# Kernel tuning notes

Hardware: AMD Instinct MI355X
Metric: run time of the kernel (lower is better)

Reference implementation:

```python
import jax, jax.numpy as jnp
import numpy as np

H, W = 128, 128  # image_shape


def setup_inputs() -> dict:
    key = jax.random.key(0)
    Y = jax.random.uniform(key, (32, H * W), dtype=jnp.float32)
    return {"Y": Y}


def reference(Y):
    # Binarize and reshape to images: [B, H, W]
    Yb = (Y > 0.5).astype(jnp.float32).reshape(-1, H, W)

    # DP over rows: heights[i, j] = number of consecutive 1s ending at row i in column j
    def step(h, row):
        h = (h + 1.0) * row
        return h, h

    _, heights = jax.lax.scan(step, jnp.zeros((Yb.shape[0], W), Yb.dtype),
                              jnp.swapaxes(Yb, 0, 1))
    heights = jnp.swapaxes(heights, 0, 1)  # [B, H, W]

    # Largest rectangle in histogram, vectorized over all rows.
    # For bar j: left[j] = prev index k with h[k] < h[j] (else -1),
    #            right[j] = next index k with h[k] < h[j] (else W).
    # This matches the monotonic-stack scan (pops while h[stack[-1]] >= h[i]).
    idx = jnp.arange(W)
    kk = idx[:, None]  # candidate index k (axis -2)
    jj = idx[None, :]  # bar index j (axis -1)
    less = heights[..., :, None] < heights[..., None, :]  # [B, H, W, W]; less[k, j] = h[k] < h[j]
    left = jnp.max(jnp.where(less & (kk < jj), kk, -1), axis=-2)   # [B, H, W]
    right = jnp.min(jnp.where(less & (kk > jj), kk, W), axis=-2)   # [B, H, W]

    area = heights * (right - left - 1).astype(heights.dtype)  # [B, H, W]
    maxarea = jnp.max(area, axis=(1, 2))  # [B]; all-zero image -> 0, matching original
    return maxarea.astype(jnp.int32)[:, None]  # [B, 1]
```

## Files before the change

kernel.cpp:

```cpp
#include <hip/hip_runtime.h>

static constexpr int H = 128;
static constexpr int W = 128;
static constexpr int B = 32;
static constexpr int RPB = 4;
static constexpr int WIN = RPB + 31;
static constexpr int GPB = H / RPB;

__global__ __launch_bounds__(64) void lr_rows(const float* __restrict__ Y,
                                              int* __restrict__ partials,
                                              int* __restrict__ out,
                                              int use_atomic) {
    const int blk = blockIdx.x;
    const int b = blk >> 5;
    const int rg = blk & (GPB - 1);
    const int r_top = rg * RPB + (RPB - 1);
    const int l = threadIdx.x;
    const float* __restrict__ yA = Y + (size_t)b * H * W + l;
    const float* __restrict__ yB = yA + 64;

    unsigned long long mA = 0ULL, mB = 0ULL;
    #pragma unroll
    for (int k = 0; k < WIN; ++k) {
        int t = r_top - k; t = t < 0 ? 0 : t;
        if (yA[(size_t)t * W] > 0.5f) mA |= (1ULL << k);
        if (yB[(size_t)t * W] > 0.5f) mB |= (1ULL << k);
    }
    if (r_top < WIN - 1) {
        const unsigned long long keep = (2ULL << r_top) - 1ULL;
        mA &= keep; mB &= keep;
    }

    int hA[RPB], hB[RPB];
    #pragma unroll
    for (int s = 0; s < RPB; ++s) {
        const int r = r_top - s;
        int a = __builtin_ctzll(~(mA >> s));
        if (a == WIN - s && r - a >= 0) {
            int t = r - a;
            while (t >= 0 && yA[(size_t)t * W] > 0.5f) { ++a; --t; }
        }
        int c = __builtin_ctzll(~(mB >> s));
        if (c == WIN - s && r - c >= 0) {
            int t = r - c;
            while (t >= 0 && yB[(size_t)t * W] > 0.5f) { ++c; --t; }
        }
        hA[s] = a; hB[s] = c;
    }

    int hm = 0;
    #pragma unroll
    for (int s = 0; s < RPB; ++s) hm = max(hm, max(hA[s], hB[s]));
    #pragma unroll
    for (int off = 32; off > 0; off >>= 1)
        hm = max(hm, __shfl_xor(hm, off, 64));

    unsigned long long loA[RPB] = {}, hiA[RPB] = {};
    unsigned long long loB[RPB] = {}, hiB[RPB] = {};
    for (int t = 1; t <= hm; ++t) {
        #pragma unroll
        for (int s = 0; s < RPB; ++s) {
            const unsigned long long lo = __ballot(hA[s] < t);
            const unsigned long long hi = __ballot(hB[s] < t);
            if (hA[s] == t) { loA[s] = lo; hiA[s] = hi; }
            if (hB[s] == t) { loB[s] = lo; hiB[s] = hi; }
        }
    }

    int acc = 0;
    #pragma unroll
    for (int s = 0; s < RPB; ++s) {
        {
            const unsigned long long below = loA[s] & ((1ULL << l) - 1ULL);
            const unsigned long long above = loA[s] & ~((2ULL << l) - 1ULL);
            const int left  = below ? 63 - __builtin_clzll(below) : -1;
            const int right = above ? __builtin_ctzll(above)
                                    : (hiA[s] ? 64 + __builtin_ctzll(hiA[s]) : W);
            acc = max(acc, hA[s] * (right - left - 1));
        }
        {
            const unsigned long long below = hiB[s] & ((1ULL << l) - 1ULL);
            const unsigned long long above = hiB[s] & ~((2ULL << l) - 1ULL);
            const int left  = below ? 64 + 63 - __builtin_clzll(below)
                                    : (loB[s] ? 63 - __builtin_clzll(loB[s]) : -1);
            const int right = above ? 64 + __builtin_ctzll(above) : W;
            acc = max(acc, hB[s] * (right - left - 1));
        }
    }

    #pragma unroll
    for (int off = 32; off > 0; off >>= 1)
        acc = max(acc, __shfl_xor(acc, off, 64));
    if (l == 0) {
        if (use_atomic) atomicMax(&out[b], acc);
        else partials[blk] = acc;
    }
}

__global__ __launch_bounds__(64) void lr_reduce(const int* __restrict__ partials,
                                                int* __restrict__ out) {
    const int b = blockIdx.x;
    const int j = threadIdx.x;
    int v = (j < GPB) ? partials[b * GPB + j] : 0;
    #pragma unroll
    for (int off = 32; off > 0; off >>= 1)
        v = max(v, __shfl_xor(v, off, 64));
    if (j == 0) out[b] = v;
}

extern "C" void kernel_launch(void* const* d_in, const int* in_sizes, int n_in,
                              void* d_out, int out_size, void* d_ws, size_t ws_size,
                              hipStream_t stream) {
    const float* Y = (const float*)d_in[0];
    int* out = (int*)d_out;

    if (ws_size >= (size_t)(B * GPB) * sizeof(int)) {
        int* partials = (int*)d_ws;
        lr_rows<<<B * GPB, 64, 0, stream>>>(Y, partials, out, 0);
        lr_reduce<<<B, 64, 0, stream>>>(partials, out);
    } else {
        hipMemsetAsync(out, 0, (size_t)out_size * sizeof(int), stream);
        lr_rows<<<B * GPB, 64, 0, stream>>>(Y, nullptr, out, 1);
    }
}
```

Measured before the change: 13.10 us.

## Fuse row kernel and reduction into one block per image with shared-memory max

Replaces the two-kernel scheme (1024 single-wave blocks writing partials, then a reduce kernel) with one kernel launching one 1024-thread block per image. Each of its 16 waves handles 8 rows, and the per-image max is combined through shared memory and __syncthreads. This removes the second launch and the global partials round trip, and halves the window overlap per row, cutting redundant loads. In exchange only 32 blocks run, so fewer CUs are used, and each wave does twice the ballot work serially.

```diff
diff --git a/kernel.cpp b/kernel.cpp
--- a/kernel.cpp
+++ b/kernel.cpp
@@ -3,19 +3,18 @@
 static constexpr int H = 128;
 static constexpr int W = 128;
 static constexpr int B = 32;
-static constexpr int RPB = 4;
-static constexpr int WIN = RPB + 31;
-static constexpr int GPB = H / RPB;
+static constexpr int RPW = 8;
+static constexpr int WIN = RPW + 31;
+static constexpr int WAVES = H / RPW;
+static constexpr int NT = WAVES * 64;
 
-__global__ __launch_bounds__(64) void lr_rows(const float* __restrict__ Y,
-                                              int* __restrict__ partials,
-                                              int* __restrict__ out,
-                                              int use_atomic) {
-    const int blk = blockIdx.x;
-    const int b = blk >> 5;
-    const int rg = blk & (GPB - 1);
-    const int r_top = rg * RPB + (RPB - 1);
-    const int l = threadIdx.x;
+__global__ __launch_bounds__(NT) void lr_batch(const float* __restrict__ Y,
+                                               int* __restrict__ out) {
+    const int b = blockIdx.x;
+    const int tid = threadIdx.x;
+    const int w = tid >> 6;
+    const int l = tid & 63;
+    const int r_top = w * RPW + (RPW - 1);
     const float* __restrict__ yA = Y + (size_t)b * H * W + l;
     const float* __restrict__ yB = yA + 64;
 
@@ -31,9 +30,9 @@
         mA &= keep; mB &= keep;
     }
 
-    int hA[RPB], hB[RPB];
+    int hA[RPW], hB[RPW];
     #pragma unroll
-    for (int s = 0; s < RPB; ++s) {
+    for (int s = 0; s < RPW; ++s) {
         const int r = r_top - s;
         int a = __builtin_ctzll(~(mA >> s));
         if (a == WIN - s && r - a >= 0) {
@@ -48,64 +47,62 @@
         hA[s] = a; hB[s] = c;
     }
 
-    int hm = 0;
+    int acc = 0;
     #pragma unroll
-    for (int s = 0; s < RPB; ++s) hm = max(hm, max(hA[s], hB[s]));
-    #pragma unroll
-    for (int off = 32; off > 0; off >>= 1)
-        hm = max(hm, __shfl_xor(hm, off, 64));
+    for (int g = 0; g < 2; ++g) {
+        const int s0 = g * 4;
+        int hm = 0;
+        #pragma unroll
+        for (int s = 0; s < 4; ++s) hm = max(hm, max(hA[s0 + s], hB[s0 + s]));
+        #pragma unroll
+        for (int off = 32; off > 0; off >>= 1)
+            hm = max(hm, __shfl_xor(hm, off, 64));
 
-    unsigned long long loA[RPB] = {}, hiA[RPB] = {};
-    unsigned long long loB[RPB] = {}, hiB[RPB] = {};
-    for (int t = 1; t <= hm; ++t) {
+        unsigned long long loA[4] = {}, hiA[4] = {};
+        unsigned long long loB[4] = {}, hiB[4] = {};
+        for (int t = 1; t <= hm; ++t) {
+            #pragma unroll
+            for (int s = 0; s < 4; ++s) {
+                const unsigned long long lo = __ballot(hA[s0 + s] < t);
+                const unsigned long long hi = __ballot(hB[s0 + s] < t);
+                if (hA[s0 + s] == t) { loA[s] = lo; hiA[s] = hi; }
+                if (hB[s0 + s] == t) { loB[s] = lo; hiB[s] = hi; }
+            }
+        }
+
         #pragma unroll
-        for (int s = 0; s < RPB; ++s) {
-            const unsigned long long lo = __ballot(hA[s] < t);
-            const unsigned long long hi = __ballot(hB[s] < t);
-            if (hA[s] == t) { loA[s] = lo; hiA[s] = hi; }
-            if (hB[s] == t) { loB[s] = lo; hiB[s] = hi; }
+        for (int s = 0; s < 4; ++s) {
+            {
+                const unsigned long long below = loA[s] & ((1ULL << l) - 1ULL);
+                const unsigned long long above = loA[s] & ~((2ULL << l) - 1ULL);
+                const int left  = below ? 63 - __builtin_clzll(below) : -1;
+                const int right = above ? __builtin_ctzll(above)
+                                        : (hiA[s] ? 64 + __builtin_ctzll(hiA[s]) : W);
+                acc = max(acc, hA[s0 + s] * (right - left - 1));
+            }
+            {
+                const unsigned long long below = hiB[s] & ((1ULL << l) - 1ULL);
+                const unsigned long long above = hiB[s] & ~((2ULL << l) - 1ULL);
+                const int left  = below ? 64 + 63 - __builtin_clzll(below)
+                                        : (loB[s] ? 63 - __builtin_clzll(loB[s]) : -1);
+                const int right = above ? 64 + __builtin_ctzll(above) : W;
+                acc = max(acc, hB[s0 + s] * (right - left - 1));
+            }
         }
     }
 
-    int acc = 0;
-    #pragma unroll
-    for (int s = 0; s < RPB; ++s) {
-        {
-            const unsigned long long below = loA[s] & ((1ULL << l) - 1ULL);
-            const unsigned long long above = loA[s] & ~((2ULL << l) - 1ULL);
-            const int left  = below ? 63 - __builtin_clzll(below) : -1;
-            const int right = above ? __builtin_ctzll(above)
-                                    : (hiA[s] ? 64 + __builtin_ctzll(hiA[s]) : W);
-            acc = max(acc, hA[s] * (right - left - 1));
-        }
-        {
-            const unsigned long long below = hiB[s] & ((1ULL << l) - 1ULL);
-            const unsigned long long above = hiB[s] & ~((2ULL << l) - 1ULL);
-            const int left  = below ? 64 + 63 - __builtin_clzll(below)
-                                    : (loB[s] ? 63 - __builtin_clzll(loB[s]) : -1);
-            const int right = above ? 64 + __builtin_ctzll(above) : W;
-            acc = max(acc, hB[s] * (right - left - 1));
-        }
-    }
-
+    __shared__ int wm[WAVES];
     #pragma unroll
     for (int off = 32; off > 0; off >>= 1)
         acc = max(acc, __shfl_xor(acc, off, 64));
-    if (l == 0) {
-        if (use_atomic) atomicMax(&out[b], acc);
-        else partials[blk] = acc;
+    if (l == 0) wm[w] = acc;
+    __syncthreads();
+    if (tid == 0) {
+        int v = wm[0];
+        #pragma unroll
+        for (int i = 1; i < WAVES; ++i) v = max(v, wm[i]);
+        out[b] = v;
     }
-}
-
-__global__ __launch_bounds__(64) void lr_reduce(const int* __restrict__ partials,
-                                                int* __restrict__ out) {
-    const int b = blockIdx.x;
-    const int j = threadIdx.x;
-    int v = (j < GPB) ? partials[b * GPB + j] : 0;
-    #pragma unroll
-    for (int off = 32; off > 0; off >>= 1)
-        v = max(v, __shfl_xor(v, off, 64));
-    if (j == 0) out[b] = v;
 }
 
 extern "C" void kernel_launch(void* const* d_in, const int* in_sizes, int n_in,
@@ -113,13 +110,7 @@
                               hipStream_t stream) {
     const float* Y = (const float*)d_in[0];
     int* out = (int*)d_out;
+    (void)d_ws; (void)ws_size;
 
-    if (ws_size >= (size_t)(B * GPB) * sizeof(int)) {
-        int* partials = (int*)d_ws;
-        lr_rows<<<B * GPB, 64, 0, stream>>>(Y, partials, out, 0);
-        lr_reduce<<<B, 64, 0, stream>>>(partials, out);
-    } else {
-        hipMemsetAsync(out, 0, (size_t)out_size * sizeof(int), stream);
-        lr_rows<<<B * GPB, 64, 0, stream>>>(Y, nullptr, out, 1);
-    }
+    lr_batch<<<B, NT, 0, stream>>>(Y, out);
 }
```

Measured after the change: 24.03 us. 83.4% more time.
